# Performance work log

Hardware: AMD Instinct MI355X
Metric: run time of the kernel (lower is better)

## Reference

```python
import jax, jax.numpy as jnp
import numpy as np
from jax import lax

NEG_SLOPE = 0.2
BN_EPS = 1e-5


def _edges(n_nodes, n_total):
    # complete graph (no self loops) on the first n_nodes nodes, as in create_complete_graph,
    # plus PyG GATConv default add_self_loops over ALL n_total nodes.
    i = np.arange(n_nodes)
    src = np.repeat(i, n_nodes)
    dst = np.tile(i, n_nodes)
    keep = src != dst
    loops = np.arange(n_total)
    src = np.concatenate([src[keep], loops]).astype(np.int32)
    dst = np.concatenate([dst[keep], loops]).astype(np.int32)
    return jnp.asarray(src), jnp.asarray(dst)


def _bn_eval(x, g, b, m, v):
    # x: [B, C, H, W]; eval-mode batchnorm with running stats
    inv = g / jnp.sqrt(v + BN_EPS)
    return x * inv[None, :, None, None] + (b - m * inv)[None, :, None, None]


def _gat(x, W, a_src, a_dst, bias, src, dst, n_total):
    h = x @ W                      # [N, D_out]
    s = h @ a_src                  # [N] per-node source score
    d = h @ a_dst                  # [N] per-node dest score
    e = jax.nn.leaky_relu(s[src] + d[dst], NEG_SLOPE)          # [E]
    emax = jax.ops.segment_max(e, dst, num_segments=n_total)   # [N]
    ex = jnp.exp(e - emax[dst])
    denom = jax.ops.segment_sum(ex, dst, num_segments=n_total)
    alpha = ex / denom[dst]                                    # [E]
    out = jax.ops.segment_sum(alpha[:, None] * h[src], dst, num_segments=n_total)
    return out + bias


def setup_inputs() -> dict:
    key = jax.random.key(0)
    ks = jax.random.split(key, 12)
    B, H, W = 8, 64, 64

    def rn(k, shape, s):
        return jax.random.normal(k, shape, jnp.float32) * s

    return {
        "images": jax.random.normal(ks[0], (B, 3, H, W), jnp.float32),
        "conv1_w": rn(ks[1], (64, 3, 3, 3), 0.1), "conv1_b": jnp.zeros((64,), jnp.float32),
        "bn1_g": jnp.ones((64,), jnp.float32), "bn1_b": jnp.zeros((64,), jnp.float32),
        "bn1_m": jnp.zeros((64,), jnp.float32), "bn1_v": jnp.ones((64,), jnp.float32),
        "conv2_w": rn(ks[2], (128, 64, 3, 3), 0.05), "conv2_b": jnp.zeros((128,), jnp.float32),
        "bn2_g": jnp.ones((128,), jnp.float32), "bn2_b": jnp.zeros((128,), jnp.float32),
        "bn2_m": jnp.zeros((128,), jnp.float32), "bn2_v": jnp.ones((128,), jnp.float32),
        "gat1_w": rn(ks[3], (128, 256), 0.05), "gat1_asrc": rn(ks[4], (256,), 0.05),
        "gat1_adst": rn(ks[5], (256,), 0.05), "gat1_bias": jnp.zeros((256,), jnp.float32),
        "gat2_w": rn(ks[6], (256, 128), 0.05), "gat2_asrc": rn(ks[7], (128,), 0.05),
        "gat2_adst": rn(ks[8], (128,), 0.05), "gat2_bias": jnp.zeros((128,), jnp.float32),
        "out_w": rn(ks[9], (128, 10), 0.05), "out_b": jnp.zeros((10,), jnp.float32),
    }


def reference(images, conv1_w, conv1_b, bn1_g, bn1_b, bn1_m, bn1_v,
              conv2_w, conv2_b, bn2_g, bn2_b, bn2_m, bn2_v,
              gat1_w, gat1_asrc, gat1_adst, gat1_bias,
              gat2_w, gat2_asrc, gat2_adst, gat2_bias,
              out_w, out_b):
    dn = ("NCHW", "OIHW", "NCHW")
    x = lax.conv_general_dilated(images, conv1_w, (1, 1), "SAME", dimension_numbers=dn)
    x = x + conv1_b[None, :, None, None]
    x = jax.nn.relu(_bn_eval(x, bn1_g, bn1_b, bn1_m, bn1_v))
    x = lax.reduce_window(x, -jnp.inf, lax.max, (1, 1, 2, 2), (1, 1, 2, 2), "VALID")
    x = lax.conv_general_dilated(x, conv2_w, (1, 1), "SAME", dimension_numbers=dn)
    x = x + conv2_b[None, :, None, None]
    x = jax.nn.relu(_bn_eval(x, bn2_g, bn2_b, bn2_m, bn2_v))

    B = x.shape[0]
    n_nodes = x.shape[2] * x.shape[3]          # (H/2)*(W/2) = 1024
    x = x.reshape(B, 128, n_nodes).transpose(0, 2, 1).reshape(-1, 128)  # [B*n, 128]
    n_total = B * n_nodes
    src, dst = _edges(n_nodes, n_total)

    x = jax.nn.relu(_gat(x, gat1_w, gat1_asrc, gat1_adst, gat1_bias, src, dst, n_total))
    x = jax.nn.relu(_gat(x, gat2_w, gat2_asrc, gat2_adst, gat2_bias, src, dst, n_total))

    x = x.reshape(B, n_nodes, 128).mean(axis=1)   # global_mean_pool over each image's nodes
    logits = x @ out_w + out_b
    return jax.nn.log_softmax(logits, axis=1)
```

## Files before the change

kernel.cpp:

```cpp
#include <hip/hip_runtime.h>
#include <math.h>

#define BN_EPS 1e-5f
#define NEG_SLOPE 0.2f

__device__ __forceinline__ float relu_f(float x) { return x > 0.f ? x : 0.f; }
__device__ __forceinline__ float leaky_f(float z) { return z > 0.f ? z : NEG_SLOPE * z; }

__global__ void conv1_pool(const float* __restrict__ img, const float* __restrict__ w,
                           const float* __restrict__ cb, const float* __restrict__ g,
                           const float* __restrict__ bb, const float* __restrict__ m,
                           const float* __restrict__ vv, float* __restrict__ out)
{
    int blk = blockIdx.x;
    int q = blk & 3, cog = (blk >> 2) & 15, b = blk >> 6;
    int t = threadIdx.x;
    int x = t & 31, y = (q << 3) + (t >> 5);

    float acc[4][4] = {};
#pragma unroll
    for (int ci = 0; ci < 3; ++ci) {
        const float* ib = img + (b * 3 + ci) * 4096;
        float rv[4][4];
#pragma unroll
        for (int r = 0; r < 4; ++r) {
            int yy = 2 * y - 1 + r;
            bool yok = (unsigned)yy < 64u;
            const float* p = ib + yy * 64 + 2 * x;
            float2 c01 = yok ? *(const float2*)p : make_float2(0.f, 0.f);
            rv[r][1] = c01.x;
            rv[r][2] = c01.y;
            rv[r][0] = (yok && x > 0) ? p[-1] : 0.f;
            rv[r][3] = (yok && x < 31) ? p[2] : 0.f;
        }
#pragma unroll
        for (int j = 0; j < 4; ++j) {
            const float* wj = w + ((cog * 4 + j) * 3 + ci) * 9;
#pragma unroll
            for (int ky = 0; ky < 3; ++ky)
#pragma unroll
                for (int kx = 0; kx < 3; ++kx) {
                    float wvv = wj[ky * 3 + kx];
#pragma unroll
                    for (int py = 0; py < 2; ++py)
#pragma unroll
                        for (int px = 0; px < 2; ++px)
                            acc[j][py * 2 + px] += rv[py + ky][px + kx] * wvv;
                }
        }
    }
#pragma unroll
    for (int j = 0; j < 4; ++j) {
        int co = cog * 4 + j;
        float inv = g[co] / sqrtf(vv[co] + BN_EPS);
        float sh = cb[co] * inv + (bb[co] - m[co] * inv);
        float v0 = relu_f(acc[j][0] * inv + sh);
        float v1 = relu_f(acc[j][1] * inv + sh);
        float v2 = relu_f(acc[j][2] * inv + sh);
        float v3 = relu_f(acc[j][3] * inv + sh);
        out[((b * 64 + co) * 32 + y) * 32 + x] = fmaxf(fmaxf(v0, v1), fmaxf(v2, v3));
    }
}

__global__ void conv2_split(const float* __restrict__ in, const float* __restrict__ w,
                            float* __restrict__ c2p)
{
    int blk = blockIdx.x;
    int kz = blk & 1, half = (blk >> 1) & 1, cog = (blk >> 2) & 31, b = blk >> 7;
    int t = threadIdx.x;
    int x2p = (t & 15) * 2;
    int y = half * 16 + (t >> 4);
    bool xnz = x2p != 0;
    bool xhi = x2p == 30;
    const float* ibase = in + b * 65536 + kz * 32768;
    int xb = xnz ? x2p - 1 : 0;

    float acc[4][2] = {};

#pragma unroll 2
    for (int ci = 0; ci < 32; ++ci) {
        const float* cb2 = ibase + ci * 1024;
        float rc[3][4];
#pragma unroll
        for (int r = 0; r < 3; ++r) {
            int yy = y - 1 + r;
            bool yok = (unsigned)yy < 32u;
            const float* p = cb2 + yy * 32 + xb;
            float4 f = yok ? *(const float4*)p : make_float4(0.f, 0.f, 0.f, 0.f);
            rc[r][0] = xnz ? f.x : 0.f;
            rc[r][1] = xnz ? f.y : f.x;
            rc[r][2] = xnz ? f.z : f.y;
            float r3 = xnz ? f.w : f.z;
            rc[r][3] = xhi ? 0.f : r3;
        }
#pragma unroll
        for (int j = 0; j < 4; ++j) {
            const float* wj = w + ((cog * 4 + j) * 64 + kz * 32 + ci) * 9;
#pragma unroll
            for (int ky = 0; ky < 3; ++ky)
#pragma unroll
                for (int kx = 0; kx < 3; ++kx) {
                    float wvv = wj[ky * 3 + kx];
                    acc[j][0] += rc[ky][kx] * wvv;
                    acc[j][1] += rc[ky][kx + 1] * wvv;
                }
        }
    }

    float* pp = c2p + (size_t)kz * 1048576;
    int bid = b * 64 + cog * 2 + half;
    size_t base = ((size_t)bid * 256 + t) * 8;
    float4 s0 = {acc[0][0], acc[1][0], acc[2][0], acc[3][0]};
    float4 s1 = {acc[0][1], acc[1][1], acc[2][1], acc[3][1]};
    *(float4*)&pp[base] = s0;
    *(float4*)&pp[base + 4] = s1;
}

__global__ void gemm1_planes(const float* __restrict__ c2p,
                             const float* __restrict__ cb, const float* __restrict__ g,
                             const float* __restrict__ bb, const float* __restrict__ mbn,
                             const float* __restrict__ vv,
                             const float* __restrict__ B, float* __restrict__ C,
                             const float* __restrict__ asrc, const float* __restrict__ adst,
                             float* __restrict__ sp, float* __restrict__ dp)
{
    __shared__ float As[16][33];
    __shared__ float Bs[16][64];
    __shared__ float invs[128];
    __shared__ float shs[128];
    int t = threadIdx.x;
    if (t < 128) {
        float iv = g[t] / sqrtf(vv[t] + BN_EPS);
        invs[t] = iv;
        shs[t] = cb[t] * iv + (bb[t] - mbn[t] * iv);
    }

    int m0 = blockIdx.x * 32;
    int n0 = blockIdx.y * 64;
    int tx = t & 15, ty = t >> 4;
    int cg = t >> 6, u = t & 63;
    int xp = u >> 2, odd = (u >> 1) & 1, j0 = (u & 1) * 2;
    int node = 2 * xp + odd;
    int kloc = cg * 4 + j0;
    int b = m0 >> 10, y = (m0 >> 5) & 31;
    int half = y >> 4, yy = y & 15;
    size_t base = (size_t)(b * 64 + half) * 2048 + yy * 128 + cg * 4096 + 2 * u;
    const float* p0 = c2p + base;
    const float* p1 = c2p + 1048576 + base;
    __syncthreads();

    float acc[2][4] = {};
    for (int k0 = 0; k0 < 128; k0 += 16) {
        float2 u0 = *(const float2*)&p0[(size_t)k0 * 1024];
        float2 u1 = *(const float2*)&p1[(size_t)k0 * 1024];
        int ch = k0 + kloc;
        float avx = relu_f((u0.x + u1.x) * invs[ch] + shs[ch]);
        float avy = relu_f((u0.y + u1.y) * invs[ch + 1] + shs[ch + 1]);
        float4 bv = *(const float4*)&B[(size_t)(k0 + ty) * 256 + n0 + tx * 4];
        __syncthreads();
        As[kloc][node] = avx;
        As[kloc + 1][node] = avy;
        *(float4*)&Bs[ty][tx * 4] = bv;
        __syncthreads();
#pragma unroll
        for (int kk = 0; kk < 16; ++kk) {
            float a0 = As[kk][ty * 2], a1 = As[kk][ty * 2 + 1];
            float4 b4 = *(const float4*)&Bs[kk][tx * 4];
            acc[0][0] += a0 * b4.x; acc[0][1] += a0 * b4.y;
            acc[0][2] += a0 * b4.z; acc[0][3] += a0 * b4.w;
            acc[1][0] += a1 * b4.x; acc[1][1] += a1 * b4.y;
            acc[1][2] += a1 * b4.z; acc[1][3] += a1 * b4.w;
        }
    }
#pragma unroll
    for (int i = 0; i < 2; ++i) {
        float4 o = {acc[i][0], acc[i][1], acc[i][2], acc[i][3]};
        *(float4*)&C[(size_t)(m0 + ty * 2 + i) * 256 + n0 + tx * 4] = o;
    }

    if (m0 < 1024) {
        float4 as4 = *(const float4*)&asrc[n0 + tx * 4];
        float4 ad4 = *(const float4*)&adst[n0 + tx * 4];
#pragma unroll
        for (int i = 0; i < 2; ++i) {
            float ss = acc[i][0] * as4.x + acc[i][1] * as4.y +
                       acc[i][2] * as4.z + acc[i][3] * as4.w;
            float dd = acc[i][0] * ad4.x + acc[i][1] * ad4.y +
                       acc[i][2] * ad4.z + acc[i][3] * ad4.w;
#pragma unroll
            for (int off = 1; off < 16; off <<= 1) {
                ss += __shfl_xor(ss, off);
                dd += __shfl_xor(dd, off);
            }
            if (tx == 0) {
                sp[blockIdx.y * 1024 + m0 + ty * 2 + i] = ss;
                dp[blockIdx.y * 1024 + m0 + ty * 2 + i] = dd;
            }
        }
    }
}

template <int K, int N, bool SELF, bool SCORE>
__global__ void gemm32(const float* __restrict__ A, const float* __restrict__ Ahi,
                       const float* __restrict__ abias,
                       const float* __restrict__ B, float* __restrict__ C,
                       const float* __restrict__ asrc, const float* __restrict__ adst,
                       float* __restrict__ sp, float* __restrict__ dp)
{
    __shared__ float As[16][33];
    __shared__ float Bs[16][64];
    int t = threadIdx.x;
    int m0 = blockIdx.x * 32;
    int n0 = blockIdx.y * 64;
    int tx = t & 15, ty = t >> 4;
    int am = t >> 3, ak2 = (t & 7) * 2;
    bool hi = SELF && m0 >= 1024;
    const float* Ab = hi ? Ahi : A;
    float acc[2][4] = {};

    for (int k0 = 0; k0 < K; k0 += 16) {
        float2 av = *(const float2*)&Ab[(size_t)(m0 + am) * K + k0 + ak2];
        if (hi) {
            av.x = relu_f(av.x + abias[k0 + ak2]);
            av.y = relu_f(av.y + abias[k0 + ak2 + 1]);
        }
        float4 bv = *(const float4*)&B[(size_t)(k0 + ty) * N + n0 + tx * 4];
        __syncthreads();
        As[ak2][am] = av.x;
        As[ak2 + 1][am] = av.y;
        *(float4*)&Bs[ty][tx * 4] = bv;
        __syncthreads();
#pragma unroll
        for (int kk = 0; kk < 16; ++kk) {
            float a0 = As[kk][ty * 2], a1 = As[kk][ty * 2 + 1];
            float4 b4 = *(const float4*)&Bs[kk][tx * 4];
            acc[0][0] += a0 * b4.x; acc[0][1] += a0 * b4.y;
            acc[0][2] += a0 * b4.z; acc[0][3] += a0 * b4.w;
            acc[1][0] += a1 * b4.x; acc[1][1] += a1 * b4.y;
            acc[1][2] += a1 * b4.z; acc[1][3] += a1 * b4.w;
        }
    }
#pragma unroll
    for (int i = 0; i < 2; ++i) {
        float4 o = {acc[i][0], acc[i][1], acc[i][2], acc[i][3]};
        *(float4*)&C[(size_t)(m0 + ty * 2 + i) * N + n0 + tx * 4] = o;
    }

    if (SCORE && m0 < 1024) {
        float4 as4 = *(const float4*)&asrc[n0 + tx * 4];
        float4 ad4 = *(const float4*)&adst[n0 + tx * 4];
#pragma unroll
        for (int i = 0; i < 2; ++i) {
            float ss = acc[i][0] * as4.x + acc[i][1] * as4.y +
                       acc[i][2] * as4.z + acc[i][3] * as4.w;
            float dd = acc[i][0] * ad4.x + acc[i][1] * ad4.y +
                       acc[i][2] * ad4.z + acc[i][3] * ad4.w;
#pragma unroll
            for (int off = 1; off < 16; off <<= 1) {
                ss += __shfl_xor(ss, off);
                dd += __shfl_xor(dd, off);
            }
            if (tx == 0) {
                sp[blockIdx.y * 1024 + m0 + ty * 2 + i] = ss;
                dp[blockIdx.y * 1024 + m0 + ty * 2 + i] = dd;
            }
        }
    }
}

template <int D, int KS, int NT>
__global__ void gat_agg_gemm(const float* __restrict__ h, const float* __restrict__ sp,
                             const float* __restrict__ dp, float* __restrict__ pacc,
                             float* __restrict__ pden)
{
    __shared__ float Ss[1024];
    __shared__ float As[16][33];
    __shared__ float Bs[16][64];
    __shared__ float red[4];
    __shared__ float part[16][32];

    const int CH = 1024 / KS;
    int t = threadIdx.x;
    int m0 = blockIdx.x * 32;
    int n0 = blockIdx.y * 64;
    int kz = blockIdx.z;
    int tx = t & 15, ty = t >> 4;
    int vg2 = tx * 2;

    float4 sa = {0.f, 0.f, 0.f, 0.f};
#pragma unroll
    for (int nt = 0; nt < NT; ++nt) {
        float4 u = *(const float4*)&sp[nt * 1024 + t * 4];
        sa.x += u.x; sa.y += u.y; sa.z += u.z; sa.w += u.w;
    }
    *(float4*)&Ss[t * 4] = sa;
    float lm = fmaxf(fmaxf(sa.x, sa.y), fmaxf(sa.z, sa.w));
#pragma unroll
    for (int off = 1; off < 64; off <<= 1) lm = fmaxf(lm, __shfl_xor(lm, off));
    if ((t & 63) == 0) red[t >> 6] = lm;
    __syncthreads();
    float smax = fmaxf(fmaxf(red[0], red[1]), fmaxf(red[2], red[3]));

    float dv0 = 0.f, dv1 = 0.f;
#pragma unroll
    for (int nt = 0; nt < NT; ++nt) {
        dv0 += dp[nt * 1024 + m0 + vg2];
        dv1 += dp[nt * 1024 + m0 + vg2 + 1];
    }
    float mv0 = leaky_f(smax + dv0), mv1 = leaky_f(smax + dv1);
    float ds0 = 0.f, ds1 = 0.f;
    float acc[2][4] = {};

    for (int k0 = kz * CH; k0 < kz * CH + CH; k0 += 16) {
        float4 bv = *(const float4*)&h[(size_t)(k0 + ty) * D + n0 + tx * 4];
        float su = Ss[k0 + ty];
        float a0 = __expf(leaky_f(su + dv0) - mv0);
        float a1 = __expf(leaky_f(su + dv1) - mv1);
        ds0 += a0; ds1 += a1;
        __syncthreads();
        As[ty][vg2] = a0;
        As[ty][vg2 + 1] = a1;
        *(float4*)&Bs[ty][tx * 4] = bv;
        __syncthreads();
#pragma unroll
        for (int kk = 0; kk < 16; ++kk) {
            float a0m = As[kk][ty * 2], a1m = As[kk][ty * 2 + 1];
            float4 b4 = *(const float4*)&Bs[kk][tx * 4];
            acc[0][0] += a0m * b4.x; acc[0][1] += a0m * b4.y;
            acc[0][2] += a0m * b4.z; acc[0][3] += a0m * b4.w;
            acc[1][0] += a1m * b4.x; acc[1][1] += a1m * b4.y;
            acc[1][2] += a1m * b4.z; acc[1][3] += a1m * b4.w;
        }
    }

    __syncthreads();
    part[ty][vg2] = ds0;
    part[ty][vg2 + 1] = ds1;
    __syncthreads();

#pragma unroll
    for (int i = 0; i < 2; ++i) {
        float4 o = {acc[i][0], acc[i][1], acc[i][2], acc[i][3]};
        *(float4*)&pacc[((size_t)kz * 1024 + m0 + ty * 2 + i) * D + n0 + tx * 4] = o;
    }
    if (t < 32) {
        float den = 0.f;
#pragma unroll
        for (int u = 0; u < 16; ++u) den += part[u][t];
        pden[kz * 1024 + m0 + t] = den;
    }
}

template <int D, int KS>
__global__ void gat_combine(const float* __restrict__ pacc, const float* __restrict__ pden,
                            const float* __restrict__ bias, float* __restrict__ out)
{
    int idx = blockIdx.x * blockDim.x + threadIdx.x;
    if (idx >= 1024 * D / 4) return;
    int c4 = idx & (D / 4 - 1);
    int v = idx / (D / 4);
    float4 a = {0.f, 0.f, 0.f, 0.f};
    float den = 0.f;
#pragma unroll
    for (int ks = 0; ks < KS; ++ks) {
        float4 p = ((const float4*)pacc)[(size_t)(ks * 1024 + v) * (D / 4) + c4];
        a.x += p.x; a.y += p.y; a.z += p.z; a.w += p.w;
        den += pden[ks * 1024 + v];
    }
    float rd = 1.f / den;
    float4 bz = ((const float4*)bias)[c4];
    float4 o = {relu_f(a.x * rd + bz.x), relu_f(a.y * rd + bz.y),
                relu_f(a.z * rd + bz.z), relu_f(a.w * rd + bz.w)};
    ((float4*)out)[(size_t)v * (D / 4) + c4] = o;
}

__global__ void pool_part(const float* __restrict__ x2, const float* __restrict__ h2,
                          const float* __restrict__ bias2, float* __restrict__ part)
{
    int b = blockIdx.x >> 4, seg = blockIdx.x & 15, t = threadIdx.x;
    float acc = 0.f;
    if (b == 0) {
        const float* p = x2 + ((size_t)seg * 64) * 128 + t;
#pragma unroll 8
        for (int n = 0; n < 64; ++n) acc += p[(size_t)n * 128];
    } else {
        float bz = bias2[t];
        const float* p = h2 + ((size_t)b * 1024 + seg * 64) * 128 + t;
#pragma unroll 8
        for (int n = 0; n < 64; ++n) acc += relu_f(p[(size_t)n * 128] + bz);
    }
    part[(b * 16 + seg) * 128 + t] = acc;
}

__global__ void head_kernel(const float* __restrict__ part, const float* __restrict__ ow,
                            const float* __restrict__ ob, float* __restrict__ out)
{
    __shared__ float pooled[128];
    __shared__ float logits[10];
    int b = blockIdx.x, t = threadIdx.x;
    float acc = 0.f;
#pragma unroll
    for (int sgi = 0; sgi < 16; ++sgi) acc += part[(b * 16 + sgi) * 128 + t];
    pooled[t] = acc * (1.f / 1024.f);
    __syncthreads();
    if (t < 10) {
        float l = ob[t];
        for (int c = 0; c < 128; ++c) l += pooled[c] * ow[c * 10 + t];
        logits[t] = l;
    }
    __syncthreads();
    if (t == 0) {
        float mx = logits[0];
        for (int j = 1; j < 10; ++j) mx = fmaxf(mx, logits[j]);
        float sum = 0.f;
        for (int j = 0; j < 10; ++j) sum += expf(logits[j] - mx);
        float lse = mx + logf(sum);
        for (int j = 0; j < 10; ++j) out[b * 10 + j] = logits[j] - lse;
    }
}

extern "C" void kernel_launch(void* const* d_in, const int* in_sizes, int n_in,
                              void* d_out, int out_size, void* d_ws, size_t ws_size,
                              hipStream_t stream)
{
    const float* images = (const float*)d_in[0];
    const float* c1w = (const float*)d_in[1];
    const float* c1b = (const float*)d_in[2];
    const float* bn1g = (const float*)d_in[3];
    const float* bn1b = (const float*)d_in[4];
    const float* bn1m = (const float*)d_in[5];
    const float* bn1v = (const float*)d_in[6];
    const float* c2w = (const float*)d_in[7];
    const float* c2b = (const float*)d_in[8];
    const float* bn2g = (const float*)d_in[9];
    const float* bn2b = (const float*)d_in[10];
    const float* bn2m = (const float*)d_in[11];
    const float* bn2v = (const float*)d_in[12];
    const float* g1w = (const float*)d_in[13];
    const float* g1as = (const float*)d_in[14];
    const float* g1ad = (const float*)d_in[15];
    const float* g1b = (const float*)d_in[16];
    const float* g2w = (const float*)d_in[17];
    const float* g2as = (const float*)d_in[18];
    const float* g2ad = (const float*)d_in[19];
    const float* g2b = (const float*)d_in[20];
    const float* ow = (const float*)d_in[21];
    const float* ob = (const float*)d_in[22];
    float* out = (float*)d_out;

    float* ws = (float*)d_ws;
    float* c2p   = ws;
    float* x1    = ws;
    float* bufc1 = ws + 2097152;
    float* h1    = ws + 2621440;
    float* pacc1 = ws + 4718592;
    float* x2    = ws + 4718592;
    float* h2    = ws + 5767168;
    float* sp1   = ws + 6815744;
    float* dp1   = ws + 6819840;
    float* sp2   = ws + 6823936;
    float* dp2   = ws + 6825984;
    float* part  = bufc1;
    float* pden1 = bufc1 + 16384;
    float* pden2 = bufc1 + 24576;
    float* pacc2 = h1;

    conv1_pool<<<512, 256, 0, stream>>>(images, c1w, c1b, bn1g, bn1b, bn1m, bn1v, bufc1);
    conv2_split<<<1024, 256, 0, stream>>>(bufc1, c2w, c2p);

    gemm1_planes<<<dim3(256, 4), 256, 0, stream>>>(
        c2p, c2b, bn2g, bn2b, bn2m, bn2v, g1w, h1, g1as, g1ad, sp1, dp1);
    gat_agg_gemm<256, 4, 4><<<dim3(32, 4, 4), 256, 0, stream>>>(h1, sp1, dp1, pacc1, pden1);
    gat_combine<256, 4><<<256, 256, 0, stream>>>(pacc1, pden1, g1b, x1);

    gemm32<256, 128, true, true><<<dim3(256, 2), 256, 0, stream>>>(
        x1, h1, g1b, g2w, h2, g2as, g2ad, sp2, dp2);
    gat_agg_gemm<128, 8, 2><<<dim3(32, 2, 8), 256, 0, stream>>>(h2, sp2, dp2, pacc2, pden2);
    gat_combine<128, 8><<<128, 256, 0, stream>>>(pacc2, pden2, g2b, x2);

    pool_part<<<128, 128, 0, stream>>>(x2, h2, g2b, part);
    head_kernel<<<8, 128, 0, stream>>>(part, ow, ob, out);
}
```

Measured before the change: 203.7 us.

## Stage full 128-deep K tiles in shared memory to cut per-step barriers

Three GEMM-style kernels now load a whole 128-row K slab of A and B into shared memory with one barrier, then run a long inner loop over it. Before, they synchronised twice every 16 K steps. In the aggregation kernel the attention weights are computed in registers per k instead of going through shared memory. This also removes the shared-memory denominator reduction, since each thread already holds the full row sum. The larger shared-memory footprint (about 25–50 KB per block) may lower occupancy, and the redundant exp work per thread grows.

```diff
diff --git a/kernel.cpp b/kernel.cpp
--- a/kernel.cpp
+++ b/kernel.cpp
@@ -124,8 +124,8 @@
                              const float* __restrict__ asrc, const float* __restrict__ adst,
                              float* __restrict__ sp, float* __restrict__ dp)
 {
-    __shared__ float As[16][33];
-    __shared__ float Bs[16][64];
+    __shared__ float As[128][33];
+    __shared__ float Bs[128][64];
     __shared__ float invs[128];
     __shared__ float shs[128];
     int t = threadIdx.x;
@@ -149,28 +149,27 @@
     const float* p1 = c2p + 1048576 + base;
     __syncthreads();
 
-    float acc[2][4] = {};
+#pragma unroll
     for (int k0 = 0; k0 < 128; k0 += 16) {
         float2 u0 = *(const float2*)&p0[(size_t)k0 * 1024];
         float2 u1 = *(const float2*)&p1[(size_t)k0 * 1024];
         int ch = k0 + kloc;
-        float avx = relu_f((u0.x + u1.x) * invs[ch] + shs[ch]);
-        float avy = relu_f((u0.y + u1.y) * invs[ch + 1] + shs[ch + 1]);
-        float4 bv = *(const float4*)&B[(size_t)(k0 + ty) * 256 + n0 + tx * 4];
-        __syncthreads();
-        As[kloc][node] = avx;
-        As[kloc + 1][node] = avy;
-        *(float4*)&Bs[ty][tx * 4] = bv;
-        __syncthreads();
-#pragma unroll
-        for (int kk = 0; kk < 16; ++kk) {
-            float a0 = As[kk][ty * 2], a1 = As[kk][ty * 2 + 1];
-            float4 b4 = *(const float4*)&Bs[kk][tx * 4];
-            acc[0][0] += a0 * b4.x; acc[0][1] += a0 * b4.y;
-            acc[0][2] += a0 * b4.z; acc[0][3] += a0 * b4.w;
-            acc[1][0] += a1 * b4.x; acc[1][1] += a1 * b4.y;
-            acc[1][2] += a1 * b4.z; acc[1][3] += a1 * b4.w;
-        }
+        As[ch][node] = relu_f((u0.x + u1.x) * invs[ch] + shs[ch]);
+        As[ch + 1][node] = relu_f((u0.y + u1.y) * invs[ch + 1] + shs[ch + 1]);
+        *(float4*)&Bs[k0 + ty][tx * 4] =
+            *(const float4*)&B[(size_t)(k0 + ty) * 256 + n0 + tx * 4];
+    }
+    __syncthreads();
+
+    float acc[2][4] = {};
+#pragma unroll 8
+    for (int k = 0; k < 128; ++k) {
+        float a0 = As[k][ty * 2], a1 = As[k][ty * 2 + 1];
+        float4 b4 = *(const float4*)&Bs[k][tx * 4];
+        acc[0][0] += a0 * b4.x; acc[0][1] += a0 * b4.y;
+        acc[0][2] += a0 * b4.z; acc[0][3] += a0 * b4.w;
+        acc[1][0] += a1 * b4.x; acc[1][1] += a1 * b4.y;
+        acc[1][2] += a1 * b4.z; acc[1][3] += a1 * b4.w;
     }
 #pragma unroll
     for (int i = 0; i < 2; ++i) {
@@ -200,40 +199,44 @@
     }
 }
 
-template <int K, int N, bool SELF, bool SCORE>
-__global__ void gemm32(const float* __restrict__ A, const float* __restrict__ Ahi,
-                       const float* __restrict__ abias,
-                       const float* __restrict__ B, float* __restrict__ C,
-                       const float* __restrict__ asrc, const float* __restrict__ adst,
-                       float* __restrict__ sp, float* __restrict__ dp)
-{
-    __shared__ float As[16][33];
-    __shared__ float Bs[16][64];
+__global__ void gemm2_sb(const float* __restrict__ A, const float* __restrict__ Ahi,
+                         const float* __restrict__ abias,
+                         const float* __restrict__ B, float* __restrict__ C,
+                         const float* __restrict__ asrc, const float* __restrict__ adst,
+                         float* __restrict__ sp, float* __restrict__ dp)
+{
+    __shared__ float As[128][33];
+    __shared__ float Bs[128][64];
     int t = threadIdx.x;
     int m0 = blockIdx.x * 32;
     int n0 = blockIdx.y * 64;
     int tx = t & 15, ty = t >> 4;
     int am = t >> 3, ak2 = (t & 7) * 2;
-    bool hi = SELF && m0 >= 1024;
+    bool hi = m0 >= 1024;
     const float* Ab = hi ? Ahi : A;
     float acc[2][4] = {};
 
-    for (int k0 = 0; k0 < K; k0 += 16) {
-        float2 av = *(const float2*)&Ab[(size_t)(m0 + am) * K + k0 + ak2];
-        if (hi) {
-            av.x = relu_f(av.x + abias[k0 + ak2]);
-            av.y = relu_f(av.y + abias[k0 + ak2 + 1]);
-        }
-        float4 bv = *(const float4*)&B[(size_t)(k0 + ty) * N + n0 + tx * 4];
+#pragma unroll
+    for (int p = 0; p < 2; ++p) {
+        if (p) __syncthreads();
+#pragma unroll
+        for (int k0 = 0; k0 < 128; k0 += 16) {
+            int kl = k0 + ak2, gk = p * 128 + kl;
+            float2 av = *(const float2*)&Ab[(size_t)(m0 + am) * 256 + gk];
+            if (hi) {
+                av.x = relu_f(av.x + abias[gk]);
+                av.y = relu_f(av.y + abias[gk + 1]);
+            }
+            As[kl][am] = av.x;
+            As[kl + 1][am] = av.y;
+            *(float4*)&Bs[k0 + ty][tx * 4] =
+                *(const float4*)&B[(size_t)(p * 128 + k0 + ty) * 128 + n0 + tx * 4];
+        }
         __syncthreads();
-        As[ak2][am] = av.x;
-        As[ak2 + 1][am] = av.y;
-        *(float4*)&Bs[ty][tx * 4] = bv;
-        __syncthreads();
-#pragma unroll
-        for (int kk = 0; kk < 16; ++kk) {
-            float a0 = As[kk][ty * 2], a1 = As[kk][ty * 2 + 1];
-            float4 b4 = *(const float4*)&Bs[kk][tx * 4];
+#pragma unroll 8
+        for (int k = 0; k < 128; ++k) {
+            float a0 = As[k][ty * 2], a1 = As[k][ty * 2 + 1];
+            float4 b4 = *(const float4*)&Bs[k][tx * 4];
             acc[0][0] += a0 * b4.x; acc[0][1] += a0 * b4.y;
             acc[0][2] += a0 * b4.z; acc[0][3] += a0 * b4.w;
             acc[1][0] += a1 * b4.x; acc[1][1] += a1 * b4.y;
@@ -243,10 +246,10 @@
 #pragma unroll
     for (int i = 0; i < 2; ++i) {
         float4 o = {acc[i][0], acc[i][1], acc[i][2], acc[i][3]};
-        *(float4*)&C[(size_t)(m0 + ty * 2 + i) * N + n0 + tx * 4] = o;
-    }
-
-    if (SCORE && m0 < 1024) {
+        *(float4*)&C[(size_t)(m0 + ty * 2 + i) * 128 + n0 + tx * 4] = o;
+    }
+
+    if (m0 < 1024) {
         float4 as4 = *(const float4*)&asrc[n0 + tx * 4];
         float4 ad4 = *(const float4*)&adst[n0 + tx * 4];
 #pragma unroll
@@ -274,10 +277,8 @@
                              float* __restrict__ pden)
 {
     __shared__ float Ss[1024];
-    __shared__ float As[16][33];
-    __shared__ float Bs[16][64];
+    __shared__ float Bs[128][64];
     __shared__ float red[4];
-    __shared__ float part[16][32];
 
     const int CH = 1024 / KS;
     int t = threadIdx.x;
@@ -311,43 +312,37 @@
     float ds0 = 0.f, ds1 = 0.f;
     float acc[2][4] = {};
 
-    for (int k0 = kz * CH; k0 < kz * CH + CH; k0 += 16) {
-        float4 bv = *(const float4*)&h[(size_t)(k0 + ty) * D + n0 + tx * 4];
-        float su = Ss[k0 + ty];
-        float a0 = __expf(leaky_f(su + dv0) - mv0);
-        float a1 = __expf(leaky_f(su + dv1) - mv1);
-        ds0 += a0; ds1 += a1;
+#pragma unroll
+    for (int p = 0; p < CH / 128; ++p) {
+        if (p) __syncthreads();
+        int kb = kz * CH + p * 128;
+#pragma unroll
+        for (int r0 = 0; r0 < 128; r0 += 16)
+            *(float4*)&Bs[r0 + ty][tx * 4] =
+                *(const float4*)&h[(size_t)(kb + r0 + ty) * D + n0 + tx * 4];
         __syncthreads();
-        As[ty][vg2] = a0;
-        As[ty][vg2 + 1] = a1;
-        *(float4*)&Bs[ty][tx * 4] = bv;
-        __syncthreads();
-#pragma unroll
-        for (int kk = 0; kk < 16; ++kk) {
-            float a0m = As[kk][ty * 2], a1m = As[kk][ty * 2 + 1];
-            float4 b4 = *(const float4*)&Bs[kk][tx * 4];
-            acc[0][0] += a0m * b4.x; acc[0][1] += a0m * b4.y;
-            acc[0][2] += a0m * b4.z; acc[0][3] += a0m * b4.w;
-            acc[1][0] += a1m * b4.x; acc[1][1] += a1m * b4.y;
-            acc[1][2] += a1m * b4.z; acc[1][3] += a1m * b4.w;
-        }
-    }
-
-    __syncthreads();
-    part[ty][vg2] = ds0;
-    part[ty][vg2 + 1] = ds1;
-    __syncthreads();
+#pragma unroll 4
+        for (int k = 0; k < 128; ++k) {
+            float su = Ss[kb + k];
+            float a0 = __expf(leaky_f(su + dv0) - mv0);
+            float a1 = __expf(leaky_f(su + dv1) - mv1);
+            ds0 += a0; ds1 += a1;
+            float4 b4 = *(const float4*)&Bs[k][tx * 4];
+            acc[0][0] += a0 * b4.x; acc[0][1] += a0 * b4.y;
+            acc[0][2] += a0 * b4.z; acc[0][3] += a0 * b4.w;
+            acc[1][0] += a1 * b4.x; acc[1][1] += a1 * b4.y;
+            acc[1][2] += a1 * b4.z; acc[1][3] += a1 * b4.w;
+        }
+    }
 
 #pragma unroll
     for (int i = 0; i < 2; ++i) {
         float4 o = {acc[i][0], acc[i][1], acc[i][2], acc[i][3]};
         *(float4*)&pacc[((size_t)kz * 1024 + m0 + ty * 2 + i) * D + n0 + tx * 4] = o;
     }
-    if (t < 32) {
-        float den = 0.f;
-#pragma unroll
-        for (int u = 0; u < 16; ++u) den += part[u][t];
-        pden[kz * 1024 + m0 + t] = den;
+    if (tx == 0) {
+        pden[kz * 1024 + m0 + ty * 2] = ds0;
+        pden[kz * 1024 + m0 + ty * 2 + 1] = ds1;
     }
 }
 
@@ -473,7 +468,7 @@
     gat_agg_gemm<256, 4, 4><<<dim3(32, 4, 4), 256, 0, stream>>>(h1, sp1, dp1, pacc1, pden1);
     gat_combine<256, 4><<<256, 256, 0, stream>>>(pacc1, pden1, g1b, x1);
 
-    gemm32<256, 128, true, true><<<dim3(256, 2), 256, 0, stream>>>(
+    gemm2_sb<<<dim3(256, 2), 256, 0, stream>>>(
         x1, h1, g1b, g2w, h2, g2as, g2ad, sp2, dp2);
     gat_agg_gemm<128, 8, 2><<<dim3(32, 2, 8), 256, 0, stream>>>(h2, sp2, dp2, pacc2, pden2);
     gat_combine<128, 8><<<128, 256, 0, stream>>>(pacc2, pden2, g2b, x2);
```

After: 217.6 us. 1.07x slower.
